# Kernel optimization log

Measured on AMD Instinct MI355X. Metric: run time of the kernel, lower is better.

The kernel has to match this reference:

```python
import jax, jax.numpy as jnp
import numpy as np

DIM = 1024
SCALE = 1.0 / np.sqrt(DIM).astype(np.float32)


def setup_inputs() -> dict:
    key = jax.random.key(0)
    ks = jax.random.split(key, 8)
    B, S, D = 4, 2048, DIM
    x = jax.random.normal(ks[0], (B, S, D), dtype=jnp.float32)
    mask = jnp.zeros((S, S), dtype=jnp.float32)  # additive mask, broadcast over batch
    # learned params (nn.Linear: y = x @ W.T + b); store W already transposed for x @ W
    init = 1.0 / np.sqrt(D)
    Wq = jax.random.uniform(ks[1], (D, D), jnp.float32, -init, init)
    bq = jax.random.uniform(ks[2], (D,), jnp.float32, -init, init)
    Wk = jax.random.uniform(ks[3], (D, D), jnp.float32, -init, init)
    bk = jax.random.uniform(ks[4], (D,), jnp.float32, -init, init)
    Wv = jax.random.uniform(ks[5], (D, D), jnp.float32, -init, init)
    bv = jax.random.uniform(ks[6], (D,), jnp.float32, -init, init)
    return {"x": x, "mask": mask, "Wq": Wq, "bq": bq, "Wk": Wk, "bk": bk, "Wv": Wv, "bv": bv}


def reference(x, mask, Wq, bq, Wk, bk, Wv, bv):
    # single-head full-dim attention, scaled by 1/sqrt(dim) (as in the source)
    q = x @ Wq + bq                      # [B, S, D]
    k = x @ Wk + bk                      # [B, S, D]
    v = x @ Wv + bv                      # [B, S, D]
    scores = jnp.einsum('bqd,bkd->bqk', q, k) * SCALE  # [B, S, S]
    scores = scores + mask               # additive mask, broadcast
    attn = jax.nn.softmax(scores, axis=-1)
    # dropout(p=0.1) is identity in eval mode
    return jnp.einsum('bqk,bkd->bqd', attn, v)  # [B, S, D]
```

## Files before the change

kernel.cpp:

```cpp
#include <hip/hip_runtime.h>

typedef unsigned short u16;
typedef unsigned int u32;

typedef __attribute__((ext_vector_type(8))) short bf16x8;
typedef __attribute__((ext_vector_type(4))) float f32x4;

static __device__ __forceinline__ u16 f2bf(float f) {
    u32 u = __float_as_uint(f);
    u32 r = (u + 0x7FFFu + ((u >> 16) & 1u)) >> 16;
    return (u16)r;
}
static __device__ __forceinline__ float bf2f(u16 h) {
    return __uint_as_float(((u32)h) << 16);
}
static __device__ __forceinline__ u32 pack2(float a, float b) {
    return (u32)f2bf(a) | ((u32)f2bf(b) << 16);
}

__global__ __launch_bounds__(256) void convert_bf16_kernel(const float* __restrict__ x,
                                                           u16* __restrict__ y, int n4) {
    int i = blockIdx.x * 256 + threadIdx.x;
    if (i < n4) {
        float4 v = ((const float4*)x)[i];
        ushort4 o;
        o.x = f2bf(v.x); o.y = f2bf(v.y); o.z = f2bf(v.z); o.w = f2bf(v.w);
        ((ushort4*)y)[i] = o;
    }
}

__global__ __launch_bounds__(256) void transpose3_to_bf16_kernel(
    const float* __restrict__ W0, const float* __restrict__ W1, const float* __restrict__ W2,
    u16* __restrict__ T0, u16* __restrict__ T1, u16* __restrict__ T2, int D) {
    __shared__ float t[32][33];
    const float* W = (blockIdx.z == 0) ? W0 : (blockIdx.z == 1) ? W1 : W2;
    u16* WT = (blockIdx.z == 0) ? T0 : (blockIdx.z == 1) ? T1 : T2;
    int bx = blockIdx.x, by = blockIdx.y;
    int tx = threadIdx.x, ty = threadIdx.y;
#pragma unroll
    for (int i = ty; i < 32; i += 8)
        t[i][tx] = W[(long)(by * 32 + i) * D + bx * 32 + tx];
    __syncthreads();
#pragma unroll
    for (int i = ty; i < 32; i += 8)
        WT[(long)(bx * 32 + i) * D + by * 32 + tx] = f2bf(t[tx][i]);
}

__global__ __launch_bounds__(256) void concat_bias_kernel(const float* __restrict__ a,
                                                          const float* __restrict__ b,
                                                          float* __restrict__ o, int n) {
    int i = blockIdx.x * 256 + threadIdx.x;
    if (i < 2 * n) o[i] = (i < n) ? a[i] : b[i - n];
}

__global__ __launch_bounds__(512, 2) void gemm256_kernel(
    const u16* __restrict__ A, int lda, long sA,
    const u16* __restrict__ B, int ldb, long sB,
    void* __restrict__ C, int ldc, long sC, int c_bf16,
    const float* __restrict__ bias, int bias_mode,
    const float* __restrict__ madd, int mask_ld,
    float* __restrict__ rowsum, int rs_mode, int rs_ld,
    float scale, int K) {
    __shared__ __align__(16) u16 SMEM[2][2 * 256 * 64];
    const int bz = blockIdx.z;
    const u16* Ab = A + (long)bz * sA;
    const u16* Bb = B + (long)bz * sB;
    int bx, by;
    {
        const int gx = gridDim.x;
        int flat = blockIdx.y * gx + blockIdx.x;
        const int cpx = (gx * gridDim.y) >> 3;
        flat = (flat & 7) * cpx + (flat >> 3);
        bx = flat % gx;
        by = flat / gx;
    }
    const int tm = by << 8, tn = bx << 8;
    const int tid = threadIdx.x, wave = tid >> 6, lane = tid & 63;
    const int wq = wave & 3;
    const int wm = (wave >> 2) << 7;
    const int wn = wq << 6;
    const int fm = lane & 15, fq = lane >> 4;
    const int T = K >> 6;

    f32x4 acc[8][4];
#pragma unroll
    for (int i = 0; i < 8; i++)
#pragma unroll
        for (int j = 0; j < 4; j++) acc[i][j] = (f32x4){0.f, 0.f, 0.f, 0.f};

    const int srow = tid >> 3;
    const int sslot = tid & 7;

    auto stageA = [&](int t, int half) {
        u16* dst = &SMEM[t & 1][0];
        const int kb = t << 6;
#pragma unroll
        for (int blk = 0; blk < 2; blk++) {
            const int r0 = blk * 128 + half * 64;
            const int r = r0 + srow;
            const int gk = kb + ((sslot ^ (r & 7)) << 3);
            const u16* ga = Ab + (long)(tm + r) * lda + gk;
            __builtin_amdgcn_global_load_lds(
                (const __attribute__((address_space(1))) void*)ga,
                (__attribute__((address_space(3))) void*)&dst[(r0 + wave * 8) * 64], 16, 0, 0);
        }
    };
    auto stageB = [&](int t, int half) {
        u16* dst = &SMEM[t & 1][256 * 64];
        const int kb = t << 6;
#pragma unroll
        for (int blk = 0; blk < 2; blk++) {
            const int r0 = half * 128 + blk * 64;
            const int r = r0 + srow;
            const int g = ((r >> 5) & 3) * 64 + (r >> 7) * 32 + (r & 31);
            const int gk = kb + ((sslot ^ (r & 7)) << 3);
            const u16* gb = Bb + (long)(tn + g) * ldb + gk;
            __builtin_amdgcn_global_load_lds(
                (const __attribute__((address_space(1))) void*)gb,
                (__attribute__((address_space(3))) void*)&dst[(r0 + wave * 8) * 64], 16, 0, 0);
        }
    };

    stageA(0, 0); stageB(0, 0); stageA(0, 1); stageB(0, 1);
    if (T > 1) {
        stageA(1, 0); stageB(1, 0); stageA(1, 1);
        asm volatile("s_waitcnt vmcnt(6)" ::: "memory");
    } else {
        asm volatile("s_waitcnt vmcnt(0)" ::: "memory");
    }
    __builtin_amdgcn_sched_barrier(0);
    __builtin_amdgcn_s_barrier();

    for (int u = 0; u < T; ++u) {
        const u16* As = &SMEM[u & 1][0];
        const u16* Bs = &SMEM[u & 1][256 * 64];
        bf16x8 alo[4][2], ahi[4][2], blo[2][2], bhi[2][2];
#pragma unroll
        for (int i = 0; i < 4; i++) {
            const int ra = wm + i * 16 + fm;
            const int sw = ra & 7;
#pragma unroll
            for (int kh = 0; kh < 2; kh++)
                alo[i][kh] = *(const bf16x8*)&As[ra * 64 + (((kh * 4 + fq) ^ sw) << 3)];
        }
#pragma unroll
        for (int j = 0; j < 2; j++) {
            const int rb = wq * 32 + j * 16 + fm;
            const int sw = rb & 7;
#pragma unroll
            for (int kh = 0; kh < 2; kh++)
                blo[j][kh] = *(const bf16x8*)&Bs[rb * 64 + (((kh * 4 + fq) ^ sw) << 3)];
        }
        if (u + 1 < T) stageB(u + 1, 1);
        __builtin_amdgcn_sched_barrier(0);
        __builtin_amdgcn_s_barrier();
        asm volatile("s_waitcnt lgkmcnt(0)" ::: "memory");
        __builtin_amdgcn_sched_barrier(0);
        __builtin_amdgcn_s_setprio(1);
#pragma unroll
        for (int kh = 0; kh < 2; kh++)
#pragma unroll
            for (int i = 0; i < 4; i++)
#pragma unroll
                for (int j = 0; j < 2; j++)
                    acc[i][j] = __builtin_amdgcn_mfma_f32_16x16x32_bf16(alo[i][kh], blo[j][kh], acc[i][j], 0, 0, 0);
        __builtin_amdgcn_s_setprio(0);
        __builtin_amdgcn_sched_barrier(0);
        __builtin_amdgcn_s_barrier();
#pragma unroll
        for (int j = 0; j < 2; j++) {
            const int rb = 128 + wq * 32 + j * 16 + fm;
            const int sw = rb & 7;
#pragma unroll
            for (int kh = 0; kh < 2; kh++)
                bhi[j][kh] = *(const bf16x8*)&Bs[rb * 64 + (((kh * 4 + fq) ^ sw) << 3)];
        }
        if (u + 2 < T) stageA(u + 2, 0);
        __builtin_amdgcn_sched_barrier(0);
        __builtin_amdgcn_s_barrier();
        asm volatile("s_waitcnt lgkmcnt(0)" ::: "memory");
        __builtin_amdgcn_sched_barrier(0);
        __builtin_amdgcn_s_setprio(1);
#pragma unroll
        for (int kh = 0; kh < 2; kh++)
#pragma unroll
            for (int i = 0; i < 4; i++)
#pragma unroll
                for (int j = 0; j < 2; j++)
                    acc[i][2 + j] = __builtin_amdgcn_mfma_f32_16x16x32_bf16(alo[i][kh], bhi[j][kh], acc[i][2 + j], 0, 0, 0);
        __builtin_amdgcn_s_setprio(0);
        __builtin_amdgcn_sched_barrier(0);
        __builtin_amdgcn_s_barrier();
#pragma unroll
        for (int i = 0; i < 4; i++) {
            const int ra = wm + 64 + i * 16 + fm;
            const int sw = ra & 7;
#pragma unroll
            for (int kh = 0; kh < 2; kh++)
                ahi[i][kh] = *(const bf16x8*)&As[ra * 64 + (((kh * 4 + fq) ^ sw) << 3)];
        }
        if (u + 2 < T) stageB(u + 2, 0);
        __builtin_amdgcn_sched_barrier(0);
        __builtin_amdgcn_s_barrier();
        asm volatile("s_waitcnt lgkmcnt(0)" ::: "memory");
        __builtin_amdgcn_sched_barrier(0);
        __builtin_amdgcn_s_setprio(1);
#pragma unroll
        for (int kh = 0; kh < 2; kh++)
#pragma unroll
            for (int i = 0; i < 4; i++)
#pragma unroll
                for (int j = 0; j < 2; j++)
                    acc[4 + i][j] = __builtin_amdgcn_mfma_f32_16x16x32_bf16(ahi[i][kh], blo[j][kh], acc[4 + i][j], 0, 0, 0);
        __builtin_amdgcn_s_setprio(0);
        __builtin_amdgcn_sched_barrier(0);
        __builtin_amdgcn_s_barrier();
        if (u + 2 < T) stageA(u + 2, 1);
        __builtin_amdgcn_s_setprio(1);
#pragma unroll
        for (int kh = 0; kh < 2; kh++)
#pragma unroll
            for (int i = 0; i < 4; i++)
#pragma unroll
                for (int j = 0; j < 2; j++)
                    acc[4 + i][2 + j] = __builtin_amdgcn_mfma_f32_16x16x32_bf16(ahi[i][kh], bhi[j][kh], acc[4 + i][2 + j], 0, 0, 0);
        __builtin_amdgcn_s_setprio(0);
        if (u + 2 < T) {
            asm volatile("s_waitcnt vmcnt(6)" ::: "memory");
        } else if (u + 1 < T) {
            asm volatile("s_waitcnt vmcnt(0)" ::: "memory");
        }
        __builtin_amdgcn_sched_barrier(0);
        __builtin_amdgcn_s_barrier();
    }
    __syncthreads();

    float* EP = (float*)&SMEM[0][0] + wave * 1088;
    const int row16 = lane >> 2, cb = (lane & 3) * 16;
    float4 bc[4];
    if (bias_mode == 1) {
#pragma unroll
        for (int q = 0; q < 4; q++) bc[q] = *(const float4*)&bias[tn + wn + cb + q * 4];
    }
#pragma unroll
    for (int i = 0; i < 8; i++) {
#pragma unroll
        for (int j = 0; j < 4; j++)
#pragma unroll
            for (int r = 0; r < 4; r++)
                EP[(fq * 4 + r) * 68 + j * 16 + fm] = acc[i][j][r];
        const long grow = tm + wm + i * 16 + row16;
        float rb = (bias_mode == 2) ? bias[grow] : 0.f;
        float4 t4[4];
#pragma unroll
        for (int q = 0; q < 4; q++) {
            float4 v = *(const float4*)&EP[row16 * 68 + cb + q * 4];
            v.x = v.x * scale + rb; v.y = v.y * scale + rb;
            v.z = v.z * scale + rb; v.w = v.w * scale + rb;
            if (bias_mode == 1) { v.x += bc[q].x; v.y += bc[q].y; v.z += bc[q].z; v.w += bc[q].w; }
            if (madd) {
                float4 m4 = *(const float4*)&madd[grow * mask_ld + tn + wn + cb + q * 4];
                v.x += m4.x; v.y += m4.y; v.z += m4.z; v.w += m4.w;
            }
            t4[q] = v;
        }
        if (rs_mode == 1) {
            float s = 0.f;
#pragma unroll
            for (int q = 0; q < 4; q++) {
                t4[q].x = __expf(t4[q].x); t4[q].y = __expf(t4[q].y);
                t4[q].z = __expf(t4[q].z); t4[q].w = __expf(t4[q].w);
                s += t4[q].x + t4[q].y + t4[q].z + t4[q].w;
            }
            s += __shfl_xor(s, 1);
            s += __shfl_xor(s, 2);
            if ((lane & 3) == 0) atomicAdd(&rowsum[(long)bz * rs_ld + grow], s);
        } else if (rs_mode == 2) {
            float inv = 1.f / rowsum[(long)bz * rs_ld + grow];
#pragma unroll
            for (int q = 0; q < 4; q++) {
                t4[q].x *= inv; t4[q].y *= inv; t4[q].z *= inv; t4[q].w *= inv;
            }
        }
        if (c_bf16) {
            u16* dst = (u16*)C + (long)bz * sC + grow * ldc + tn + wn + cb;
            uint4 o0 = {pack2(t4[0].x, t4[0].y), pack2(t4[0].z, t4[0].w),
                        pack2(t4[1].x, t4[1].y), pack2(t4[1].z, t4[1].w)};
            uint4 o1 = {pack2(t4[2].x, t4[2].y), pack2(t4[2].z, t4[2].w),
                        pack2(t4[3].x, t4[3].y), pack2(t4[3].z, t4[3].w)};
            *(uint4*)dst = o0;
            *(uint4*)(dst + 8) = o1;
        } else {
            float* dst = (float*)C + (long)bz * sC + grow * ldc + tn + wn + cb;
#pragma unroll
            for (int q = 0; q < 4; q++) *(float4*)(dst + q * 4) = t4[q];
        }
    }
}

__global__ __launch_bounds__(256, 4) void gemm_bt_kernel(
    const u16* __restrict__ A, int lda, long sA,
    const u16* __restrict__ B, int ldb, long sB,
    void* __restrict__ C, int ldc, long sC, int c_bf16,
    const float* __restrict__ bias, int bias_mode,
    const float* __restrict__ madd, int mask_ld,
    float* __restrict__ rowsum, int rs_mode, int rs_ld, int swapxy,
    float scale, int K) {
    __shared__ __align__(16) u16 SMEM[2][256 * 32];
    const int bz = blockIdx.z;
    const u16* Ab = A + (long)bz * sA;
    const u16* Bb = B + (long)bz * sB;
    const int bxi = swapxy ? blockIdx.y : blockIdx.x;
    const int byi = swapxy ? blockIdx.x : blockIdx.y;
    const int tm = byi * 128, tn = bxi * 128;
    const int tid = threadIdx.x, wave = tid >> 6, lane = tid & 63;
    const int wm = (wave >> 1) * 64, wn = (wave & 1) * 64;
    const int lr = lane >> 2, c = lane & 3;
    const int fm = lane & 15, fq = lane >> 4;

    f32x4 acc[4][4];
#pragma unroll
    for (int i = 0; i < 4; i++)
#pragma unroll
        for (int j = 0; j < 4; j++) acc[i][j] = (f32x4){0.f, 0.f, 0.f, 0.f};

    const int T = K >> 5;

    auto stage = [&](int t, int buf) {
        u16* As = &SMEM[buf][0];
        u16* Bs = &SMEM[buf][128 * 32];
#pragma unroll
        for (int r = 0; r < 2; r++) {
            const int rl = r * 64 + wave * 16;
            const int row = rl + lr;
            const int kc = (t << 5) + ((c ^ ((row ^ (row >> 2)) & 3)) << 3);
            const u16* ga = Ab + (long)(tm + row) * lda + kc;
            const u16* gb = Bb + (long)(tn + row) * ldb + kc;
            __builtin_amdgcn_global_load_lds((const __attribute__((address_space(1))) void*)ga,
                                             (__attribute__((address_space(3))) void*)&As[rl * 32],
                                             16, 0, 0);
            __builtin_amdgcn_global_load_lds((const __attribute__((address_space(1))) void*)gb,
                                             (__attribute__((address_space(3))) void*)&Bs[rl * 32],
                                             16, 0, 0);
        }
    };

    stage(0, 0);
    __syncthreads();
    for (int t = 0; t < T; t++) {
        const int cur = t & 1;
        if (t + 1 < T) stage(t + 1, cur ^ 1);
        const u16* As = &SMEM[cur][0];
        const u16* Bs = &SMEM[cur][128 * 32];
        bf16x8 af[4], bfr[4];
#pragma unroll
        for (int i = 0; i < 4; i++) {
            int row = wm + i * 16 + fm;
            af[i] = *(const bf16x8*)&As[row * 32 + ((fq ^ ((row ^ (row >> 2)) & 3)) << 3)];
        }
#pragma unroll
        for (int j = 0; j < 4; j++) {
            int row = wn + j * 16 + fm;
            bfr[j] = *(const bf16x8*)&Bs[row * 32 + ((fq ^ ((row ^ (row >> 2)) & 3)) << 3)];
        }
#pragma unroll
        for (int i = 0; i < 4; i++)
#pragma unroll
            for (int j = 0; j < 4; j++)
                acc[i][j] = __builtin_amdgcn_mfma_f32_16x16x32_bf16(af[i], bfr[j], acc[i][j], 0, 0, 0);
        if (t + 1 < T) __syncthreads();
    }
    __syncthreads();

    float* EP = (float*)&SMEM[0][0] + wave * 1088;
    const int row16 = lane >> 2, cb = (lane & 3) * 16;
    float4 bc[4];
    if (bias_mode == 1) {
#pragma unroll
        for (int q = 0; q < 4; q++) bc[q] = *(const float4*)&bias[tn + wn + cb + q * 4];
    }
#pragma unroll
    for (int i = 0; i < 4; i++) {
#pragma unroll
        for (int j = 0; j < 4; j++)
#pragma unroll
            for (int r = 0; r < 4; r++)
                EP[(fq * 4 + r) * 68 + j * 16 + fm] = acc[i][j][r];
        const long grow = tm + wm + i * 16 + row16;
        float rb = (bias_mode == 2) ? bias[grow] : 0.f;
        float4 t4[4];
#pragma unroll
        for (int q = 0; q < 4; q++) {
            float4 v = *(const float4*)&EP[row16 * 68 + cb + q * 4];
            v.x = v.x * scale + rb; v.y = v.y * scale + rb;
            v.z = v.z * scale + rb; v.w = v.w * scale + rb;
            if (bias_mode == 1) { v.x += bc[q].x; v.y += bc[q].y; v.z += bc[q].z; v.w += bc[q].w; }
            if (madd) {
                float4 m4 = *(const float4*)&madd[grow * mask_ld + tn + wn + cb + q * 4];
                v.x += m4.x; v.y += m4.y; v.z += m4.z; v.w += m4.w;
            }
            t4[q] = v;
        }
        if (rs_mode == 1) {
            float s = 0.f;
#pragma unroll
            for (int q = 0; q < 4; q++) {
                t4[q].x = __expf(t4[q].x); t4[q].y = __expf(t4[q].y);
                t4[q].z = __expf(t4[q].z); t4[q].w = __expf(t4[q].w);
                s += t4[q].x + t4[q].y + t4[q].z + t4[q].w;
            }
            s += __shfl_xor(s, 1);
            s += __shfl_xor(s, 2);
            if ((lane & 3) == 0) atomicAdd(&rowsum[(long)bz * rs_ld + grow], s);
        } else if (rs_mode == 2) {
            float inv = 1.f / rowsum[(long)bz * rs_ld + grow];
#pragma unroll
            for (int q = 0; q < 4; q++) {
                t4[q].x *= inv; t4[q].y *= inv; t4[q].z *= inv; t4[q].w *= inv;
            }
        }
        if (c_bf16) {
            u16* dst = (u16*)C + (long)bz * sC + grow * ldc + tn + wn + cb;
            uint4 o0 = {pack2(t4[0].x, t4[0].y), pack2(t4[0].z, t4[0].w),
                        pack2(t4[1].x, t4[1].y), pack2(t4[1].z, t4[1].w)};
            uint4 o1 = {pack2(t4[2].x, t4[2].y), pack2(t4[2].z, t4[2].w),
                        pack2(t4[3].x, t4[3].y), pack2(t4[3].z, t4[3].w)};
            *(uint4*)dst = o0;
            *(uint4*)(dst + 8) = o1;
        } else {
            float* dst = (float*)C + (long)bz * sC + grow * ldc + tn + wn + cb;
#pragma unroll
            for (int q = 0; q < 4; q++) *(float4*)(dst + q * 4) = t4[q];
        }
    }
}

extern "C" void kernel_launch(void* const* d_in, const int* in_sizes, int n_in,
                              void* d_out, int out_size, void* d_ws, size_t ws_size,
                              hipStream_t stream) {
    const float* x    = (const float*)d_in[0];
    const float* mask = (const float*)d_in[1];
    const float* Wq   = (const float*)d_in[2];
    const float* bq   = (const float*)d_in[3];
    const float* Wk   = (const float*)d_in[4];
    const float* bk   = (const float*)d_in[5];
    const float* Wv   = (const float*)d_in[6];
    const float* bv   = (const float*)d_in[7];
    float* out = (float*)d_out;

    const int B = 4, S = 2048, D = 1024;
    const long MS = (long)B * S;

    size_t need = (size_t)MS * D * 2 + (size_t)(2 * D) * D * 2 + (size_t)D * D * 2
                + (size_t)(2 * D) * 4 + (size_t)MS * (2 * D) * 2 + (size_t)D * MS * 2
                + (size_t)B * S * S * 2 + (size_t)B * S * 4;
    if (ws_size < need) return;

    char* ws = (char*)d_ws;
    u16*  xb   = (u16*)ws;  ws += (long)MS * D * 2;
    u16*  wqkt = (u16*)ws;  ws += (long)(2 * D) * D * 2;
    u16*  wvt  = (u16*)ws;  ws += (long)D * D * 2;
    float* bqk = (float*)ws; ws += (long)(2 * D) * 4;
    u16*  QK   = (u16*)ws;  ws += (long)MS * (2 * D) * 2;
    u16*  VT   = (u16*)ws;  ws += (long)D * MS * 2;
    u16*  sc   = (u16*)ws;  ws += (long)B * S * S * 2;
    float* rsum = (float*)ws; ws += (long)B * S * 4;

    const float SCALE = 0.03125f;

    hipMemsetAsync(rsum, 0, (size_t)B * S * 4, stream);

    convert_bf16_kernel<<<(int)((MS * D / 4 + 255) / 256), 256, 0, stream>>>(x, xb, (int)(MS * D / 4));
    transpose3_to_bf16_kernel<<<dim3(32, 32, 3), dim3(32, 8), 0, stream>>>(
        Wq, Wk, Wv, wqkt, wqkt + (long)D * D, wvt, D);
    concat_bias_kernel<<<8, 256, 0, stream>>>(bq, bk, bqk, D);

    gemm256_kernel<<<dim3(2 * D / 256, (int)(MS / 256), 1), 512, 0, stream>>>(
        xb, D, 0, wqkt, D, 0, QK, 2 * D, 0, 1, bqk, 1, nullptr, 0,
        nullptr, 0, 0, 1.0f, D);
    gemm_bt_kernel<<<dim3((int)(MS / 128), D / 128, 1), 256, 0, stream>>>(
        wvt, D, 0, xb, D, 0, VT, (int)MS, 0, 1, bv, 2, nullptr, 0,
        nullptr, 0, 0, 0, 1.0f, D);

    gemm256_kernel<<<dim3(S / 256, S / 256, B), 512, 0, stream>>>(
        QK, 2 * D, (long)S * 2 * D, QK + D, 2 * D, (long)S * 2 * D, sc, S, (long)S * S, 1,
        nullptr, 0, mask, S, rsum, 1, S, SCALE, D);

    gemm_bt_kernel<<<dim3(S / 128, D / 128, B), 256, 0, stream>>>(
        sc, S, (long)S * S, VT, (int)MS, (long)S, out, D, (long)S * D, 0,
        nullptr, 0, nullptr, 0, rsum, 2, S, 1, 1.0f, S);
}
```

Baseline: 276.2 us.

## Software-pipeline LDS fragment reads across MFMA phases in bf16 GEMM loop

Restructures the GEMM main loop so LDS fragment reads for the next phase are issued before the current phase's MFMAs, and the next tile's alo/blo fragments are prefetched during the final MFMA block. It removes the explicit lgkmcnt(0) waits and several barriers between phases, leaving the compiler to insert the LDS waits. The goal is to hide LDS read latency behind matrix-core work. The costs are extra register pressure from holding prefetched fragments, and a more delicate synchronisation order around the double-buffered shared memory.

```diff
diff --git a/kernel.cpp b/kernel.cpp
--- a/kernel.cpp
+++ b/kernel.cpp
@@ -121,6 +121,27 @@
         }
     };
 
+    auto read_a4 = [&](const u16* Ls, bf16x8 (&d)[4][2], int base) {
+#pragma unroll
+        for (int i = 0; i < 4; i++) {
+            const int ra = base + i * 16 + fm;
+            const int sw = ra & 7;
+#pragma unroll
+            for (int kh = 0; kh < 2; kh++)
+                d[i][kh] = *(const bf16x8*)&Ls[ra * 64 + (((kh * 4 + fq) ^ sw) << 3)];
+        }
+    };
+    auto read_b2 = [&](const u16* Ls, bf16x8 (&d)[2][2], int base) {
+#pragma unroll
+        for (int j = 0; j < 2; j++) {
+            const int rb = base + j * 16 + fm;
+            const int sw = rb & 7;
+#pragma unroll
+            for (int kh = 0; kh < 2; kh++)
+                d[j][kh] = *(const bf16x8*)&Ls[rb * 64 + (((kh * 4 + fq) ^ sw) << 3)];
+        }
+    };
+
     stageA(0, 0); stageB(0, 0); stageA(0, 1); stageB(0, 1);
     if (T > 1) {
         stageA(1, 0); stageB(1, 0); stageA(1, 1);
@@ -130,31 +151,19 @@
     }
     __builtin_amdgcn_sched_barrier(0);
     __builtin_amdgcn_s_barrier();
+    __builtin_amdgcn_sched_barrier(0);
+
+    bf16x8 alo[4][2], ahi[4][2], blo[2][2], bhi[2][2];
+    read_a4(&SMEM[0][0], alo, wm);
+    read_b2(&SMEM[0][256 * 64], blo, wq * 32);
 
     for (int u = 0; u < T; ++u) {
         const u16* As = &SMEM[u & 1][0];
         const u16* Bs = &SMEM[u & 1][256 * 64];
-        bf16x8 alo[4][2], ahi[4][2], blo[2][2], bhi[2][2];
-#pragma unroll
-        for (int i = 0; i < 4; i++) {
-            const int ra = wm + i * 16 + fm;
-            const int sw = ra & 7;
-#pragma unroll
-            for (int kh = 0; kh < 2; kh++)
-                alo[i][kh] = *(const bf16x8*)&As[ra * 64 + (((kh * 4 + fq) ^ sw) << 3)];
-        }
-#pragma unroll
-        for (int j = 0; j < 2; j++) {
-            const int rb = wq * 32 + j * 16 + fm;
-            const int sw = rb & 7;
-#pragma unroll
-            for (int kh = 0; kh < 2; kh++)
-                blo[j][kh] = *(const bf16x8*)&Bs[rb * 64 + (((kh * 4 + fq) ^ sw) << 3)];
-        }
+        const u16* As2 = &SMEM[(u + 1) & 1][0];
+        const u16* Bs2 = &SMEM[(u + 1) & 1][256 * 64];
         if (u + 1 < T) stageB(u + 1, 1);
-        __builtin_amdgcn_sched_barrier(0);
-        __builtin_amdgcn_s_barrier();
-        asm volatile("s_waitcnt lgkmcnt(0)" ::: "memory");
+        read_b2(Bs, bhi, 128 + wq * 32);
         __builtin_amdgcn_sched_barrier(0);
         __builtin_amdgcn_s_setprio(1);
 #pragma unroll
@@ -167,18 +176,9 @@
         __builtin_amdgcn_s_setprio(0);
         __builtin_amdgcn_sched_barrier(0);
         __builtin_amdgcn_s_barrier();
-#pragma unroll
-        for (int j = 0; j < 2; j++) {
-            const int rb = 128 + wq * 32 + j * 16 + fm;
-            const int sw = rb & 7;
-#pragma unroll
-            for (int kh = 0; kh < 2; kh++)
-                bhi[j][kh] = *(const bf16x8*)&Bs[rb * 64 + (((kh * 4 + fq) ^ sw) << 3)];
-        }
+        __builtin_amdgcn_sched_barrier(0);
         if (u + 2 < T) stageA(u + 2, 0);
-        __builtin_amdgcn_sched_barrier(0);
-        __builtin_amdgcn_s_barrier();
-        asm volatile("s_waitcnt lgkmcnt(0)" ::: "memory");
+        read_a4(As, ahi, wm + 64);
         __builtin_amdgcn_sched_barrier(0);
         __builtin_amdgcn_s_setprio(1);
 #pragma unroll
@@ -191,18 +191,8 @@
         __builtin_amdgcn_s_setprio(0);
         __builtin_amdgcn_sched_barrier(0);
         __builtin_amdgcn_s_barrier();
-#pragma unroll
-        for (int i = 0; i < 4; i++) {
-            const int ra = wm + 64 + i * 16 + fm;
-            const int sw = ra & 7;
-#pragma unroll
-            for (int kh = 0; kh < 2; kh++)
-                ahi[i][kh] = *(const bf16x8*)&As[ra * 64 + (((kh * 4 + fq) ^ sw) << 3)];
-        }
+        __builtin_amdgcn_sched_barrier(0);
         if (u + 2 < T) stageB(u + 2, 0);
-        __builtin_amdgcn_sched_barrier(0);
-        __builtin_amdgcn_s_barrier();
-        asm volatile("s_waitcnt lgkmcnt(0)" ::: "memory");
         __builtin_amdgcn_sched_barrier(0);
         __builtin_amdgcn_s_setprio(1);
 #pragma unroll
@@ -215,7 +205,21 @@
         __builtin_amdgcn_s_setprio(0);
         __builtin_amdgcn_sched_barrier(0);
         __builtin_amdgcn_s_barrier();
-        if (u + 2 < T) stageA(u + 2, 1);
+        __builtin_amdgcn_sched_barrier(0);
+        if (u + 2 < T) {
+            stageA(u + 2, 1);
+            asm volatile("s_waitcnt vmcnt(6)" ::: "memory");
+        } else {
+            asm volatile("s_waitcnt vmcnt(0)" ::: "memory");
+        }
+        __builtin_amdgcn_sched_barrier(0);
+        __builtin_amdgcn_s_barrier();
+        __builtin_amdgcn_sched_barrier(0);
+        if (u + 1 < T) {
+            read_a4(As2, alo, wm);
+            read_b2(Bs2, blo, wq * 32);
+        }
+        __builtin_amdgcn_sched_barrier(0);
         __builtin_amdgcn_s_setprio(1);
 #pragma unroll
         for (int kh = 0; kh < 2; kh++)
@@ -225,13 +229,6 @@
                 for (int j = 0; j < 2; j++)
                     acc[4 + i][2 + j] = __builtin_amdgcn_mfma_f32_16x16x32_bf16(ahi[i][kh], bhi[j][kh], acc[4 + i][2 + j], 0, 0, 0);
         __builtin_amdgcn_s_setprio(0);
-        if (u + 2 < T) {
-            asm volatile("s_waitcnt vmcnt(6)" ::: "memory");
-        } else if (u + 1 < T) {
-            asm volatile("s_waitcnt vmcnt(0)" ::: "memory");
-        }
-        __builtin_amdgcn_sched_barrier(0);
-        __builtin_amdgcn_s_barrier();
     }
     __syncthreads();
 
```

Result: no change. 279.0 us (+1.0%).
